# Kernel optimization log

Measured on AMD Instinct MI355X. Metric: run time of the kernel, lower is better.

Reference implementation:

```python
import jax, jax.numpy as jnp
import numpy as np

EPS = 1e-8  # torch cosine_similarity clamps norms at 1e-8
TEMPERATURE = 0.05


def _normalize(x):
    n = jnp.linalg.norm(x, axis=-1, keepdims=True)
    return x / jnp.maximum(n, EPS)


def setup_inputs() -> dict:
    key = jax.random.key(0)
    k1, k2, k3 = jax.random.split(key, 3)
    N, D = 8192, 256
    return {
        "text_embeddings": jax.random.normal(k1, (N, D), dtype=jnp.float32),
        "text_pos_embeddings": jax.random.normal(k2, (N, D), dtype=jnp.float32),
        "text_neg_embeddings": jax.random.normal(k3, (N, D), dtype=jnp.float32),
    }


def _pair_loss(a, b):
    # PairInBatchNegCoSentLoss(a, b): cos-sim matrix, scale, diag-subtract, LSE
    sim = _normalize(a) @ _normalize(b).T / TEMPERATURE  # [N, N]
    diff = sim - jnp.diagonal(sim)[:, None]
    return jax.nn.logsumexp(diff, axis=1).mean()


def reference(text_embeddings, text_pos_embeddings, text_neg_embeddings):
    e = _normalize(text_embeddings)
    p = _normalize(text_pos_embeddings)
    n = _normalize(text_neg_embeddings)
    sim_pos = jnp.sum(e * p, axis=-1)          # [N]
    sim_neg = e @ n.T                          # [N, N]
    sim = jnp.concatenate([sim_pos[:, None], sim_neg], axis=1) / TEMPERATURE
    diff = sim - sim[:, 0:1]
    loss = jax.nn.logsumexp(diff, axis=1).mean()
    # add_swap_loss=True: pair loss with (pos, anchor) swapped
    loss = loss + _pair_loss(text_pos_embeddings, text_embeddings)
    return loss
```

## Files before the change

### kernel.cpp

```cpp
#include <hip/hip_runtime.h>
#include <stdint.h>

#define N 8192
#define D 256
#define INV_T 20.0f
#define LOG2E 1.44269504088896340736f
#define BM 128
#define BN 128
#define NCHUNK 4
#define NT 16

typedef __attribute__((ext_vector_type(16))) float f32x16;
typedef __attribute__((ext_vector_type(4))) int i32x4;
typedef __attribute__((ext_vector_type(8))) int i32x8;

typedef __attribute__((address_space(3))) uint32_t lds_u32;
typedef __attribute__((address_space(1))) const uint32_t gbl_u32;

static __device__ __forceinline__ float fast_exp2(float x) {
  float r;
  asm("v_exp_f32 %0, %1" : "=v"(r) : "v"(x));
  return r;
}

__global__ __launch_bounds__(256) void normalize_kernel(
    const float* __restrict__ e, const float* __restrict__ p, const float* __restrict__ n,
    uint32_t* __restrict__ eb, uint32_t* __restrict__ pb, uint32_t* __restrict__ nb,
    float* __restrict__ cbuf, float* __restrict__ out) {
  const int tid = threadIdx.x;
  const int wave = tid >> 6, lane = tid & 63;
  const int row = blockIdx.x * 4 + wave;

  if (blockIdx.x == 0 && tid == 0) out[0] = 0.0f;

  const float4 ev = ((const float4*)(e + (size_t)row * D))[lane];
  const float4 pv = ((const float4*)(p + (size_t)row * D))[lane];
  const float4 nv = ((const float4*)(n + (size_t)row * D))[lane];

  float sse = ev.x*ev.x + ev.y*ev.y + ev.z*ev.z + ev.w*ev.w;
  float ssp = pv.x*pv.x + pv.y*pv.y + pv.z*pv.z + pv.w*pv.w;
  float ssn = nv.x*nv.x + nv.y*nv.y + nv.z*nv.z + nv.w*nv.w;
  float dep = ev.x*pv.x + ev.y*pv.y + ev.z*pv.z + ev.w*pv.w;
#pragma unroll
  for (int m = 1; m < 64; m <<= 1) {
    sse += __shfl_xor(sse, m);
    ssp += __shfl_xor(ssp, m);
    ssn += __shfl_xor(ssn, m);
    dep += __shfl_xor(dep, m);
  }
  const float se = 1.0f / fmaxf(sqrtf(sse), 1e-8f);
  const float sp = 1.0f / fmaxf(sqrtf(ssp), 1e-8f);
  const float sn = 1.0f / fmaxf(sqrtf(ssn), 1e-8f);

  int ue = __builtin_amdgcn_cvt_pk_fp8_f32(ev.x*se, ev.y*se, 0, false);
  ue     = __builtin_amdgcn_cvt_pk_fp8_f32(ev.z*se, ev.w*se, ue, true);
  int up = __builtin_amdgcn_cvt_pk_fp8_f32(pv.x*sp, pv.y*sp, 0, false);
  up     = __builtin_amdgcn_cvt_pk_fp8_f32(pv.z*sp, pv.w*sp, up, true);
  int un = __builtin_amdgcn_cvt_pk_fp8_f32(nv.x*sn, nv.y*sn, 0, false);
  un     = __builtin_amdgcn_cvt_pk_fp8_f32(nv.z*sn, nv.w*sn, un, true);
  eb[row * 64 + lane] = (uint32_t)ue;
  pb[row * 64 + lane] = (uint32_t)up;
  nb[row * 64 + lane] = (uint32_t)un;

  if (lane == 0) cbuf[row] = dep * se * sp * INV_T;
}

__global__ __launch_bounds__(256, 2) void simexp_kernel(
    const uint8_t* __restrict__ eb, const uint8_t* __restrict__ pb,
    const uint8_t* __restrict__ nb, const float* __restrict__ cbuf,
    float* __restrict__ part) {
  __shared__ uint8_t Bs[2][BN * D];

  const int z = blockIdx.z;
  const uint8_t* __restrict__ A = z ? pb : eb;
  const uint8_t* __restrict__ B = z ? eb : nb;

  const int tid = threadIdx.x;
  const int wave = tid >> 6, lane = tid & 63;
  const int lane31 = lane & 31, half = lane >> 5;
  const int chunk = blockIdx.x;
  const int rowTile = blockIdx.y * BM;
  const int colblk0 = chunk * NT;

#define STAGEB(buf, cblk)                                                     \
  do {                                                                        \
    const uint8_t* __restrict__ Bsrc = B + (size_t)(cblk) * (BN * D);         \
    _Pragma("unroll") for (int i = 0; i < 8; ++i) {                           \
      const int c = i * 256 + tid, r = c >> 4, sl = c & 15;                   \
      const int gg = sl ^ (r & 15);                                           \
      __builtin_amdgcn_global_load_lds(                                       \
          (gbl_u32*)(Bsrc + (size_t)r * D + gg * 16),                         \
          (lds_u32*)&Bs[buf][c * 16], 16, 0, 0);                              \
    }                                                                         \
  } while (0)

  const int arow = rowTile + wave * 32 + lane31;
  const uint8_t* __restrict__ Arow = A + (size_t)arow * D + half * 32;
  i32x8 afr[4];
#pragma unroll
  for (int s = 0; s < 4; ++s) {
    const i32x4 lo = *(const i32x4*)(Arow + s * 64);
    const i32x4 hi = *(const i32x4*)(Arow + s * 64 + 16);
    afr[s] = (i32x8){lo[0], lo[1], lo[2], lo[3], hi[0], hi[1], hi[2], hi[3]};
  }
  const float cv = cbuf[arow] * LOG2E;
  __builtin_amdgcn_sched_barrier(0);
  STAGEB(0, colblk0 + 0);
  STAGEB(1, colblk0 + 1);
  __builtin_amdgcn_sched_barrier(0);

  int bbase[4];
#pragma unroll
  for (int ni = 0; ni < 4; ++ni) {
    const int cl = ni * 32 + lane31;
    bbase[ni] = (cl << 8) ^ ((cl & 15) << 4) ^ (half << 5);
  }

  const float K2 = INV_T * LOG2E;
  float sacc0 = 0.0f, sacc1 = 0.0f, sacc2 = 0.0f, sacc3 = 0.0f;

#pragma unroll 1
  for (int t = 0; t < NT; ++t) {
    if (t < NT - 1) asm volatile("s_waitcnt vmcnt(8)" ::: "memory");
    else            asm volatile("s_waitcnt vmcnt(0)" ::: "memory");
    __builtin_amdgcn_s_barrier();
    __builtin_amdgcn_sched_barrier(0);

    const int bpar = (t & 1) << 15;
    f32x16 acc[4];
#pragma unroll
    for (int ni = 0; ni < 4; ++ni)
#pragma unroll
      for (int r = 0; r < 16; ++r) acc[ni][r] = 0.0f;

#pragma unroll
    for (int s = 0; s < 4; ++s) {
#pragma unroll
      for (int ni = 0; ni < 4; ++ni) {
        const int alo = (bbase[ni] ^ bpar) ^ (s << 6);
        const i32x4 blo = *(const i32x4*)&Bs[0][alo];
        const i32x4 bhi = *(const i32x4*)&Bs[0][alo ^ 16];
        const i32x8 b = (i32x8){blo[0], blo[1], blo[2], blo[3],
                                bhi[0], bhi[1], bhi[2], bhi[3]};
        acc[ni] = __builtin_amdgcn_mfma_scale_f32_32x32x64_f8f6f4(
            b, afr[s], acc[ni],
            0 , 0 ,
            0, 0x7F7F7F7F , 0, 0x7F7F7F7F );
      }
    }

    __builtin_amdgcn_sched_barrier(0);
    __builtin_amdgcn_s_barrier();
    __builtin_amdgcn_sched_barrier(0);

    if (t + 2 < NT) STAGEB(t & 1, colblk0 + t + 2);

#pragma unroll
    for (int reg = 0; reg < 16; ++reg) {
      sacc0 += fast_exp2(acc[0][reg] * K2 - cv);
      sacc1 += fast_exp2(acc[1][reg] * K2 - cv);
      sacc2 += fast_exp2(acc[2][reg] * K2 - cv);
      sacc3 += fast_exp2(acc[3][reg] * K2 - cv);
    }
  }
#undef STAGEB

  float v = (sacc0 + sacc1) + (sacc2 + sacc3);
  v += __shfl_xor(v, 32);
  if (lane < 32)
    part[((size_t)(z * NCHUNK + chunk)) * N + rowTile + wave * 32 + lane] = v;
}

__global__ __launch_bounds__(64) void finalize_kernel(const float* __restrict__ part,
                                                      float* __restrict__ out) {
  const int r = blockIdx.x * 64 + threadIdx.x;
  const int z = r >> 13, row = r & (N - 1);
  const float* __restrict__ base = part + (size_t)(z * NCHUNK) * N + row;
  float s0 = base[0];
  float s1 = base[(size_t)1 * N];
  float s2 = base[(size_t)2 * N];
  float s3 = base[(size_t)3 * N];
  const float s = (s0 + s1) + (s2 + s3);
  float val = z ? logf(s) : log1pf(s);
#pragma unroll
  for (int m = 1; m < 64; m <<= 1) val += __shfl_xor(val, m);
  if (threadIdx.x == 0) atomicAdd(out, val * (1.0f / (float)N));
}

extern "C" void kernel_launch(void* const* d_in, const int* in_sizes, int n_in,
                              void* d_out, int out_size, void* d_ws, size_t ws_size,
                              hipStream_t stream) {
  const float* e = (const float*)d_in[0];
  const float* p = (const float*)d_in[1];
  const float* n = (const float*)d_in[2];

  char* w = (char*)d_ws;
  uint8_t* eb = (uint8_t*)w;
  uint8_t* pb = eb + (size_t)N * D;
  uint8_t* nb = pb + (size_t)N * D;
  float* cbuf = (float*)(nb + (size_t)N * D);
  float* part = cbuf + N;

  normalize_kernel<<<N / 4, 256, 0, stream>>>(e, p, n, (uint32_t*)eb, (uint32_t*)pb,
                                              (uint32_t*)nb, cbuf, (float*)d_out);
  simexp_kernel<<<dim3(NCHUNK, N / BM, 2), 256, 0, stream>>>(eb, pb, nb, cbuf, part);
  finalize_kernel<<<256, 64, 0, stream>>>(part, (float*)d_out);
}
```

Baseline: 117.5 us.

## Use 2x2 wave tiling in simexp to halve LDS B-fragment reads

Each wave previously covered 32 rows × 128 columns and read all four B column fragments from shared memory per k-step. Waves are now arranged 2×2, each covering 64 rows × 64 columns, so each loaded B fragment feeds two MFMAs and LDS read traffic per wave is halved. The cost is doubled A-fragment registers and an extra shared-memory reduction with a block barrier to combine the two column halves per row at the end.

```diff
diff --git a/kernel.cpp b/kernel.cpp
--- a/kernel.cpp
+++ b/kernel.cpp
@@ -70,6 +70,7 @@
     const uint8_t* __restrict__ nb, const float* __restrict__ cbuf,
     float* __restrict__ part) {
   __shared__ uint8_t Bs[2][BN * D];
+  __shared__ float sm[2][BM];
 
   const int z = blockIdx.z;
   const uint8_t* __restrict__ A = z ? pb : eb;
@@ -78,6 +79,7 @@
   const int tid = threadIdx.x;
   const int wave = tid >> 6, lane = tid & 63;
   const int lane31 = lane & 31, half = lane >> 5;
+  const int wr = wave >> 1, wc = wave & 1;
   const int chunk = blockIdx.x;
   const int rowTile = blockIdx.y * BM;
   const int colblk0 = chunk * NT;
@@ -94,30 +96,36 @@
     }                                                                         \
   } while (0)
 
-  const int arow = rowTile + wave * 32 + lane31;
-  const uint8_t* __restrict__ Arow = A + (size_t)arow * D + half * 32;
-  i32x8 afr[4];
-#pragma unroll
-  for (int s = 0; s < 4; ++s) {
-    const i32x4 lo = *(const i32x4*)(Arow + s * 64);
-    const i32x4 hi = *(const i32x4*)(Arow + s * 64 + 16);
-    afr[s] = (i32x8){lo[0], lo[1], lo[2], lo[3], hi[0], hi[1], hi[2], hi[3]};
-  }
-  const float cv = cbuf[arow] * LOG2E;
+  i32x8 afr[2][4];
+  float cv[2];
+#pragma unroll
+  for (int rg = 0; rg < 2; ++rg) {
+    const int arow = rowTile + wr * 64 + rg * 32 + lane31;
+    const uint8_t* __restrict__ Arow = A + (size_t)arow * D + half * 32;
+#pragma unroll
+    for (int s = 0; s < 4; ++s) {
+      const i32x4 lo = *(const i32x4*)(Arow + s * 64);
+      const i32x4 hi = *(const i32x4*)(Arow + s * 64 + 16);
+      afr[rg][s] = (i32x8){lo[0], lo[1], lo[2], lo[3], hi[0], hi[1], hi[2], hi[3]};
+    }
+    cv[rg] = cbuf[arow] * LOG2E;
+  }
   __builtin_amdgcn_sched_barrier(0);
   STAGEB(0, colblk0 + 0);
   STAGEB(1, colblk0 + 1);
   __builtin_amdgcn_sched_barrier(0);
 
-  int bbase[4];
-#pragma unroll
-  for (int ni = 0; ni < 4; ++ni) {
-    const int cl = ni * 32 + lane31;
-    bbase[ni] = (cl << 8) ^ ((cl & 15) << 4) ^ (half << 5);
+  int bbase[2];
+#pragma unroll
+  for (int cg = 0; cg < 2; ++cg) {
+    const int cl = wc * 64 + cg * 32 + lane31;
+    bbase[cg] = (cl << 8) ^ ((cl & 15) << 4) ^ (half << 5);
   }
 
   const float K2 = INV_T * LOG2E;
-  float sacc0 = 0.0f, sacc1 = 0.0f, sacc2 = 0.0f, sacc3 = 0.0f;
+  float sacc[4];
+#pragma unroll
+  for (int i = 0; i < 4; ++i) sacc[i] = 0.0f;
 
 #pragma unroll 1
   for (int t = 0; t < NT; ++t) {
@@ -127,26 +135,33 @@
     __builtin_amdgcn_sched_barrier(0);
 
     const int bpar = (t & 1) << 15;
-    f32x16 acc[4];
-#pragma unroll
-    for (int ni = 0; ni < 4; ++ni)
-#pragma unroll
-      for (int r = 0; r < 16; ++r) acc[ni][r] = 0.0f;
+    f32x16 acc[2][2];
+#pragma unroll
+    for (int rg = 0; rg < 2; ++rg)
+#pragma unroll
+      for (int cg = 0; cg < 2; ++cg)
+#pragma unroll
+        for (int r = 0; r < 16; ++r) acc[rg][cg][r] = 0.0f;
 
 #pragma unroll
     for (int s = 0; s < 4; ++s) {
-#pragma unroll
-      for (int ni = 0; ni < 4; ++ni) {
-        const int alo = (bbase[ni] ^ bpar) ^ (s << 6);
+      i32x8 b[2];
+#pragma unroll
+      for (int cg = 0; cg < 2; ++cg) {
+        const int alo = (bbase[cg] ^ bpar) ^ (s << 6);
         const i32x4 blo = *(const i32x4*)&Bs[0][alo];
         const i32x4 bhi = *(const i32x4*)&Bs[0][alo ^ 16];
-        const i32x8 b = (i32x8){blo[0], blo[1], blo[2], blo[3],
-                                bhi[0], bhi[1], bhi[2], bhi[3]};
-        acc[ni] = __builtin_amdgcn_mfma_scale_f32_32x32x64_f8f6f4(
-            b, afr[s], acc[ni],
-            0 , 0 ,
-            0, 0x7F7F7F7F , 0, 0x7F7F7F7F );
+        b[cg] = (i32x8){blo[0], blo[1], blo[2], blo[3],
+                        bhi[0], bhi[1], bhi[2], bhi[3]};
       }
+#pragma unroll
+      for (int rg = 0; rg < 2; ++rg)
+#pragma unroll
+        for (int cg = 0; cg < 2; ++cg)
+          acc[rg][cg] = __builtin_amdgcn_mfma_scale_f32_32x32x64_f8f6f4(
+              b[cg], afr[rg][s], acc[rg][cg],
+              0 , 0 ,
+              0, 0x7F7F7F7F , 0, 0x7F7F7F7F );
     }
 
     __builtin_amdgcn_sched_barrier(0);
@@ -157,18 +172,26 @@
 
 #pragma unroll
     for (int reg = 0; reg < 16; ++reg) {
-      sacc0 += fast_exp2(acc[0][reg] * K2 - cv);
-      sacc1 += fast_exp2(acc[1][reg] * K2 - cv);
-      sacc2 += fast_exp2(acc[2][reg] * K2 - cv);
-      sacc3 += fast_exp2(acc[3][reg] * K2 - cv);
+      sacc[0] += fast_exp2(acc[0][0][reg] * K2 - cv[0]);
+      sacc[1] += fast_exp2(acc[0][1][reg] * K2 - cv[0]);
+      sacc[2] += fast_exp2(acc[1][0][reg] * K2 - cv[1]);
+      sacc[3] += fast_exp2(acc[1][1][reg] * K2 - cv[1]);
     }
   }
 #undef STAGEB
 
-  float v = (sacc0 + sacc1) + (sacc2 + sacc3);
-  v += __shfl_xor(v, 32);
-  if (lane < 32)
-    part[((size_t)(z * NCHUNK + chunk)) * N + rowTile + wave * 32 + lane] = v;
+  float v0 = sacc[0] + sacc[1];
+  float v1 = sacc[2] + sacc[3];
+  v0 += __shfl_xor(v0, 32);
+  v1 += __shfl_xor(v1, 32);
+  if (lane < 32) {
+    sm[wc][wr * 64 + lane] = v0;
+    sm[wc][wr * 64 + 32 + lane] = v1;
+  }
+  __syncthreads();
+  if (tid < BM)
+    part[((size_t)(z * NCHUNK + chunk)) * N + rowTile + tid] =
+        sm[0][tid] + sm[1][tid];
 }
 
 __global__ __launch_bounds__(64) void finalize_kernel(const float* __restrict__ part,
```

Result: faster. 115.0 us (-2.1%).
